# Kernel tuning notes

Hardware: AMD Instinct MI355X
Metric: run time of the kernel (lower is better)

Reference implementation:

```python
import jax, jax.numpy as jnp
import numpy as np

INPUT_DIM = 64
HIDDEN_DIM = 32


def setup_inputs() -> dict:
    key = jax.random.key(0)
    ks = jax.random.split(key, 9)
    B, C, H, W = 8, INPUT_DIM, 64, 64
    s_in = 1.0 / np.sqrt(C)
    inp = {
        "h": jax.random.normal(ks[0], (B, C, H, W), dtype=jnp.float32),
        # 1x1 conv weights stored as [out, in]
        "wq": jax.random.uniform(ks[1], (HIDDEN_DIM, C), jnp.float32, -s_in, s_in),
        "bq": jax.random.uniform(ks[2], (HIDDEN_DIM,), jnp.float32, -s_in, s_in),
        "wk": jax.random.uniform(ks[3], (HIDDEN_DIM, C), jnp.float32, -s_in, s_in),
        "bk": jax.random.uniform(ks[4], (HIDDEN_DIM,), jnp.float32, -s_in, s_in),
        "wv": jax.random.uniform(ks[5], (C, C), jnp.float32, -s_in, s_in),
        "bv": jax.random.uniform(ks[6], (C,), jnp.float32, -s_in, s_in),
        "wz": jax.random.uniform(ks[7], (C, C), jnp.float32, -s_in, s_in),
        "bz": jax.random.uniform(ks[8], (C,), jnp.float32, -s_in, s_in),
    }
    return inp


def reference(h, wq, bq, wk, bk, wv, bv, wz, bz):
    B, C, H, W = h.shape
    N = H * W
    x = h.reshape(B, C, N)  # [B, C, N]
    # 1x1 convs == channel-wise linear maps
    q = jnp.einsum('oc,bcn->bno', wq, x) + bq          # [B, N, Dh]
    k = jnp.einsum('oc,bcn->bon', wk, x) + bk[:, None]  # [B, Dh, N]
    v = jnp.einsum('oc,bcn->bon', wv, x) + bv[:, None]  # [B, C, N]
    attn = jax.nn.softmax(jnp.einsum('bnd,bdm->bnm', q, k), axis=-1)  # [B, N, N]
    z = jnp.einsum('bnm,bcm->bcn', attn, v)             # [B, C, N]
    out = jnp.einsum('oc,bcn->bon', wz, z) + bz[:, None]
    return out.reshape(B, C, H, W) + h
```

## Files before the change

kernel.cpp:

```cpp
#include <hip/hip_runtime.h>
#include <stdint.h>

#define BATCH 8
#define CIN   64
#define DH    32
#define NTOK  4096
#define LOG2E 1.4426950408889634f

typedef float    f4   __attribute__((ext_vector_type(4)));
typedef short    s8v  __attribute__((ext_vector_type(8)));
typedef uint32_t u32;
typedef uint32_t u32x2 __attribute__((ext_vector_type(2)));
typedef uint32_t u32x4 __attribute__((ext_vector_type(4)));

static __device__ __forceinline__ short f2bf(float f) {
    union { float f; u32 u; } c; c.f = f;
    u32 u = c.u;
    u32 r = (u + 0x7fffu + ((u >> 16) & 1u)) >> 16;
    return (short)(r & 0xffffu);
}
static __device__ __forceinline__ u32 pk2(float a, float b) {
    return (u32)(uint16_t)f2bf(a) | ((u32)(uint16_t)f2bf(b) << 16);
}
static __device__ __forceinline__ u32 pktr(float a, float b) {
    union { float f; u32 u; } ca, cb; ca.f = a; cb.f = b;
#if __has_builtin(__builtin_amdgcn_perm)
    return __builtin_amdgcn_perm(cb.u, ca.u, 0x07060302u);
#else
    return (cb.u & 0xffff0000u) | (ca.u >> 16);
#endif
}
static __device__ __forceinline__ float bfhi(u32 u) {
    union { u32 u; float f; } c; c.u = u & 0xffff0000u; return c.f;
}
static __device__ __forceinline__ float bflo(u32 u) {
    union { u32 u; float f; } c; c.u = u << 16; return c.f;
}

__global__ __launch_bounds__(256) void proj_kernel(
    const float* __restrict__ h,
    const float* __restrict__ wq, const float* __restrict__ bq,
    const float* __restrict__ wk, const float* __restrict__ bk,
    const float* __restrict__ wv, const float* __restrict__ bv,
    short* __restrict__ qbf, short* __restrict__ kbf, short* __restrict__ vp)
{
    __shared__ short xT [64 * 72];
    __shared__ short wqs[32 * 72];
    __shared__ short wks[32 * 72];
    __shared__ short wvs[64 * 72];
    __shared__ short vls2[64 * 68];
    __shared__ float bqs[32], bks[32], bvs[64];

    const int t   = threadIdx.x;
    const int b   = blockIdx.x;
    const int nt0 = blockIdx.y * 64;

    {
        const int c  = t >> 2;
        const int ng = (t & 3) * 16;
        const float* src = h + ((size_t)(b * CIN + c)) * NTOK + nt0 + ng;
        f4 x0 = *(const f4*)(src + 0);
        f4 x1 = *(const f4*)(src + 4);
        f4 x2 = *(const f4*)(src + 8);
        f4 x3 = *(const f4*)(src + 12);
        #pragma unroll
        for (int i = 0; i < 4; ++i) {
            xT[(ng + 0  + i) * 72 + c] = f2bf(x0[i]);
            xT[(ng + 4  + i) * 72 + c] = f2bf(x1[i]);
            xT[(ng + 8  + i) * 72 + c] = f2bf(x2[i]);
            xT[(ng + 12 + i) * 72 + c] = f2bf(x3[i]);
        }
    }
    for (int idx = t; idx < 2048; idx += 256) {
        int o = idx >> 6, c = idx & 63;
        wqs[o * 72 + c] = f2bf(wq[idx] * LOG2E);
        wks[o * 72 + c] = f2bf(wk[idx]);
    }
    for (int idx = t; idx < 4096; idx += 256)
        wvs[(idx >> 6) * 72 + (idx & 63)] = f2bf(wv[idx]);
    if (t < 32) { bqs[t] = bq[t] * LOG2E; bks[t] = bk[t]; }
    if (t < 64) bvs[t] = bv[t];
    __syncthreads();

    const int w    = t >> 6;
    const int ln   = t & 15;
    const int quad = (t >> 4) & 3;
    const int nl   = w * 16 + ln;
    const int n    = nt0 + nl;
    const f4 zf4 = {0.f, 0.f, 0.f, 0.f};

    const s8v xb0 = *(const s8v*)&xT[nl * 72 + quad * 8];
    const s8v xb1 = *(const s8v*)&xT[nl * 72 + 32 + quad * 8];

    #pragma unroll
    for (int ot = 0; ot < 2; ++ot) {
        s8v a0 = *(const s8v*)&wqs[(ot * 16 + ln) * 72 + quad * 8];
        s8v a1 = *(const s8v*)&wqs[(ot * 16 + ln) * 72 + 32 + quad * 8];
        f4 d = __builtin_amdgcn_mfma_f32_16x16x32_bf16(a0, xb0, zf4, 0, 0, 0);
        d     = __builtin_amdgcn_mfma_f32_16x16x32_bf16(a1, xb1, d,  0, 0, 0);
        f4 bb = *(const f4*)&bqs[ot * 16 + quad * 4];
        u32x2 pw; pw[0] = pk2(d[0] + bb[0], d[1] + bb[1]);
                  pw[1] = pk2(d[2] + bb[2], d[3] + bb[3]);
        *(u32x2*)(qbf + ((size_t)(b * NTOK + n)) * DH + ot * 16 + quad * 4) = pw;

        s8v c0 = *(const s8v*)&wks[(ot * 16 + ln) * 72 + quad * 8];
        s8v c1 = *(const s8v*)&wks[(ot * 16 + ln) * 72 + 32 + quad * 8];
        f4 e = __builtin_amdgcn_mfma_f32_16x16x32_bf16(c0, xb0, zf4, 0, 0, 0);
        e     = __builtin_amdgcn_mfma_f32_16x16x32_bf16(c1, xb1, e,  0, 0, 0);
        f4 kb = *(const f4*)&bks[ot * 16 + quad * 4];
        u32x2 kw; kw[0] = pk2(e[0] + kb[0], e[1] + kb[1]);
                  kw[1] = pk2(e[2] + kb[2], e[3] + kb[3]);
        *(u32x2*)(kbf + ((size_t)(b * NTOK + n)) * DH + ot * 16 + quad * 4) = kw;
    }

    {
        const int p    = nl & 31;
        const int row  = (nl >> 5) * 32 + ((p >> 2) & 3) * 8
                       + (p >> 4) * 4 + (p & 3);
        short* vrow = &vls2[row * 68];
        #pragma unroll
        for (int ot = 0; ot < 4; ++ot) {
            s8v a0 = *(const s8v*)&wvs[(ot * 16 + ln) * 72 + quad * 8];
            s8v a1 = *(const s8v*)&wvs[(ot * 16 + ln) * 72 + 32 + quad * 8];
            f4 d = __builtin_amdgcn_mfma_f32_16x16x32_bf16(a0, xb0, zf4, 0, 0, 0);
            d     = __builtin_amdgcn_mfma_f32_16x16x32_bf16(a1, xb1, d,  0, 0, 0);
            const int ch = ot * 16 + quad * 4;
            u32x2 pw;
            pw[0] = pk2(d[0] + bvs[ch],     d[1] + bvs[ch + 1]);
            pw[1] = pk2(d[2] + bvs[ch + 2], d[3] + bvs[ch + 3]);
            *(u32x2*)&vrow[ch] = pw;
        }
    }
    __syncthreads();

    {
        const int g = t >> 5;
        const int r = t & 31;
        short tmp[16];
        #pragma unroll
        for (int j = 0; j < 8; ++j)
            #pragma unroll
            for (int cc = 0; cc < 2; ++cc)
                tmp[cc * 8 + j] = vls2[(g * 8 + j) * 68 + r * 2 + cc];
        u32x4* dst = (u32x4*)(vp + ((size_t)(b * 128 + blockIdx.y * 2) * 4) * 64 * 8);
        #pragma unroll
        for (int i = 0; i < 2; ++i)
            dst[t * 2 + i] = ((const u32x4*)tmp)[i];
    }
}

__global__ __launch_bounds__(256, 2) void attn_kernel(
    const float* __restrict__ h,  const float* __restrict__ wz,
    const float* __restrict__ bz,
    const short* __restrict__ qbf, const short* __restrict__ kbf,
    const short* __restrict__ vp,  float* __restrict__ out)
{
    __shared__ short accb[4][64][72];
    __shared__ short zbuf[64][72];
    __shared__ float lbuf[4][64];

    const int b    = blockIdx.x;
    const int qb0  = blockIdx.y * 64;
    const int tid  = threadIdx.x;
    const int w    = tid >> 6;
    const int lane = tid & 63;
    const int ln   = lane & 15;
    const int quad = lane >> 4;
    const f4 zf4 = {0.f, 0.f, 0.f, 0.f};

    s8v qf[4];
    #pragma unroll
    for (int f = 0; f < 4; ++f)
        qf[f] = *(const s8v*)(qbf + ((size_t)(b * NTOK + qb0 + f * 16 + ln)) * DH + quad * 8);

    f4 acc[4][4];
    f4 accl[4];
    #pragma unroll
    for (int f = 0; f < 4; ++f) {
        accl[f] = zf4;
        #pragma unroll
        for (int ct = 0; ct < 4; ++ct) acc[f][ct] = zf4;
    }
    s8v ones;
    #pragma unroll
    for (int j = 0; j < 8; ++j) ones[j] = (short)0x3F80;

    const short* kb2 = kbf + ((size_t)b * NTOK + w * 1024) * DH;
    const s8v*   vb2 = (const s8v*)(vp + (size_t)b * NTOK * CIN)
                     + (size_t)(w * 32) * 4 * 64;

    for (int kt = 0; kt < 1024; kt += 32) {
        const short* kp = kb2 + kt * DH;
        s8v kk0 = *(const s8v*)(kp + ln * DH + quad * 8);
        s8v kk1 = *(const s8v*)(kp + (16 + ln) * DH + quad * 8);
        const s8v* vg = vb2 + (size_t)((kt >> 5) * 4 + quad) * 64 + ln;
        s8v v0 = vg[0], v1 = vg[16], v2 = vg[32], v3 = vg[48];

        #pragma unroll
        for (int f = 0; f < 4; ++f) {
            f4 sa = __builtin_amdgcn_mfma_f32_16x16x32_bf16(kk0, qf[f], zf4, 0, 0, 0);
            f4 sb = __builtin_amdgcn_mfma_f32_16x16x32_bf16(kk1, qf[f], zf4, 0, 0, 0);
            f4 ea, eb;
            #pragma unroll
            for (int r = 0; r < 4; ++r) {
                ea[r] = __builtin_amdgcn_exp2f(sa[r]);
                eb[r] = __builtin_amdgcn_exp2f(sb[r]);
            }
            u32x4 pd;
            pd[0] = pktr(ea[0], ea[1]); pd[1] = pktr(ea[2], ea[3]);
            pd[2] = pktr(eb[0], eb[1]); pd[3] = pktr(eb[2], eb[3]);
            s8v pf = __builtin_bit_cast(s8v, pd);

            accl[f]   = __builtin_amdgcn_mfma_f32_16x16x32_bf16(ones, pf, accl[f],   0, 0, 0);
            acc[f][0] = __builtin_amdgcn_mfma_f32_16x16x32_bf16(v0,   pf, acc[f][0], 0, 0, 0);
            acc[f][1] = __builtin_amdgcn_mfma_f32_16x16x32_bf16(v1,   pf, acc[f][1], 0, 0, 0);
            acc[f][2] = __builtin_amdgcn_mfma_f32_16x16x32_bf16(v2,   pf, acc[f][2], 0, 0, 0);
            acc[f][3] = __builtin_amdgcn_mfma_f32_16x16x32_bf16(v3,   pf, acc[f][3], 0, 0, 0);
        }
    }

    if (quad == 0) {
        #pragma unroll
        for (int f = 0; f < 4; ++f) lbuf[w][f * 16 + ln] = accl[f][0];
    }
    #pragma unroll
    for (int f = 0; f < 4; ++f) {
        #pragma unroll
        for (int ct = 0; ct < 4; ++ct) {
            u32x2 pw;
            pw[0] = pk2(acc[f][ct][0], acc[f][ct][1]);
            pw[1] = pk2(acc[f][ct][2], acc[f][ct][3]);
            *(u32x2*)&accb[w][f * 16 + ln][ct * 16 + quad * 4] = pw;
        }
    }
    __syncthreads();

    {
        const int q   = tid >> 2;
        const int chg = (tid & 3) * 16;
        float ls = lbuf[0][q] + lbuf[1][q] + lbuf[2][q] + lbuf[3][q];
        float rl = __builtin_amdgcn_rcpf(ls);
        float zv[16];
        #pragma unroll
        for (int i = 0; i < 16; ++i) zv[i] = 0.f;
        #pragma unroll
        for (int w2 = 0; w2 < 4; ++w2) {
            u32x4 ua = *(u32x4*)&accb[w2][q][chg];
            u32x4 ub = *(u32x4*)&accb[w2][q][chg + 8];
            #pragma unroll
            for (int d = 0; d < 4; ++d) {
                zv[d * 2]     += bflo(ua[d]); zv[d * 2 + 1]     += bfhi(ua[d]);
                zv[8 + d * 2] += bflo(ub[d]); zv[8 + d * 2 + 1] += bfhi(ub[d]);
            }
        }
        u32x4 za, zb2;
        #pragma unroll
        for (int d = 0; d < 4; ++d) {
            za[d]  = pk2(zv[d * 2] * rl,     zv[d * 2 + 1] * rl);
            zb2[d] = pk2(zv[8 + d * 2] * rl, zv[8 + d * 2 + 1] * rl);
        }
        *(u32x4*)&zbuf[q][chg]     = za;
        *(u32x4*)&zbuf[q][chg + 8] = zb2;
    }
    __syncthreads();

    {
        const int ot = w;
        s8v wzf[2];
        #pragma unroll
        for (int half = 0; half < 2; ++half) {
            const float* wp = wz + (ot * 16 + ln) * 64 + half * 32 + quad * 8;
            f4 wa = *(const f4*)wp;
            f4 wb = *(const f4*)(wp + 4);
            u32x4 tt;
            tt[0] = pk2(wa[0], wa[1]); tt[1] = pk2(wa[2], wa[3]);
            tt[2] = pk2(wb[0], wb[1]); tt[3] = pk2(wb[2], wb[3]);
            wzf[half] = __builtin_bit_cast(s8v, tt);
        }
        f4 bzv = *(const f4*)(bz + ot * 16 + quad * 4);
        #pragma unroll
        for (int fi = 0; fi < 4; ++fi) {
            const int row = fi * 16 + ln;
            s8v z0 = *(const s8v*)&zbuf[row][quad * 8];
            s8v z1 = *(const s8v*)&zbuf[row][32 + quad * 8];
            f4 oa = __builtin_amdgcn_mfma_f32_16x16x32_bf16(wzf[0], z0, zf4, 0, 0, 0);
            oa     = __builtin_amdgcn_mfma_f32_16x16x32_bf16(wzf[1], z1, oa,  0, 0, 0);
            #pragma unroll
            for (int r = 0; r < 4; ++r) {
                size_t idx = ((size_t)(b * CIN + ot * 16 + quad * 4 + r)) * NTOK
                           + qb0 + row;
                out[idx] = oa[r] + bzv[r] + h[idx];
            }
        }
    }
}

extern "C" void kernel_launch(void* const* d_in, const int* in_sizes, int n_in,
                              void* d_out, int out_size, void* d_ws, size_t ws_size,
                              hipStream_t stream) {
    (void)in_sizes; (void)n_in; (void)out_size; (void)ws_size;
    const float* h  = (const float*)d_in[0];
    const float* wq = (const float*)d_in[1];
    const float* bq = (const float*)d_in[2];
    const float* wk = (const float*)d_in[3];
    const float* bk = (const float*)d_in[4];
    const float* wv = (const float*)d_in[5];
    const float* bv = (const float*)d_in[6];
    const float* wz = (const float*)d_in[7];
    const float* bz = (const float*)d_in[8];
    float* out = (float*)d_out;

    short* qbf = (short*)d_ws;
    short* kbf = qbf + (size_t)BATCH * NTOK * DH;
    short* vpw = kbf + (size_t)BATCH * NTOK * DH;

    proj_kernel<<<dim3(8, 64), dim3(256), 0, stream>>>(
        h, wq, bq, wk, bk, wv, bv, qbf, kbf, vpw);
    attn_kernel<<<dim3(8, 64), dim3(256), 0, stream>>>(
        h, wz, bz, qbf, kbf, vpw, out);
}
```

Before: 117.2 us.

## Double-buffer K/V register loads in attention loop and vectorize weight staging

```diff
diff --git a/kernel.cpp b/kernel.cpp
--- a/kernel.cpp
+++ b/kernel.cpp
@@ -71,13 +71,24 @@
             xT[(ng + 12 + i) * 72 + c] = f2bf(x3[i]);
         }
     }
-    for (int idx = t; idx < 2048; idx += 256) {
-        int o = idx >> 6, c = idx & 63;
-        wqs[o * 72 + c] = f2bf(wq[idx] * LOG2E);
-        wks[o * 72 + c] = f2bf(wk[idx]);
-    }
-    for (int idx = t; idx < 4096; idx += 256)
-        wvs[(idx >> 6) * 72 + (idx & 63)] = f2bf(wv[idx]);
+    #pragma unroll
+    for (int idx = t; idx < 512; idx += 256) {
+        f4 a = *(const f4*)(wq + idx * 4);
+        f4 c = *(const f4*)(wk + idx * 4);
+        const int o = idx >> 4, cc = (idx & 15) * 4;
+        u32x2 qa; qa[0] = pk2(a[0] * LOG2E, a[1] * LOG2E);
+                  qa[1] = pk2(a[2] * LOG2E, a[3] * LOG2E);
+        u32x2 ka; ka[0] = pk2(c[0], c[1]); ka[1] = pk2(c[2], c[3]);
+        *(u32x2*)&wqs[o * 72 + cc] = qa;
+        *(u32x2*)&wks[o * 72 + cc] = ka;
+    }
+    #pragma unroll
+    for (int idx = t; idx < 1024; idx += 256) {
+        f4 a = *(const f4*)(wv + idx * 4);
+        const int o = idx >> 4, cc = (idx & 15) * 4;
+        u32x2 va; va[0] = pk2(a[0], a[1]); va[1] = pk2(a[2], a[3]);
+        *(u32x2*)&wvs[o * 72 + cc] = va;
+    }
     if (t < 32) { bqs[t] = bq[t] * LOG2E; bks[t] = bk[t]; }
     if (t < 64) bvs[t] = bv[t];
     __syncthreads();
@@ -149,6 +160,47 @@
     }
 }
 
+static __device__ __forceinline__ void load_kv(
+    const short* __restrict__ kb2, const s8v* __restrict__ vb2,
+    int kt, int ln, int quad,
+    s8v& kk0, s8v& kk1, s8v& v0, s8v& v1, s8v& v2, s8v& v3)
+{
+    const short* kp = kb2 + kt * DH;
+    kk0 = *(const s8v*)(kp + ln * DH + quad * 8);
+    kk1 = *(const s8v*)(kp + (16 + ln) * DH + quad * 8);
+    const s8v* vg = vb2 + (size_t)((kt >> 5) * 4 + quad) * 64 + ln;
+    v0 = vg[0]; v1 = vg[16]; v2 = vg[32]; v3 = vg[48];
+}
+
+static __device__ __forceinline__ void attn_step(
+    const s8v& kk0, const s8v& kk1,
+    const s8v& v0, const s8v& v1, const s8v& v2, const s8v& v3,
+    const s8v (&qf)[4], const s8v& ones, f4 (&acc)[4][4], f4 (&accl)[4])
+{
+    const f4 zf4 = {0.f, 0.f, 0.f, 0.f};
+    #pragma unroll
+    for (int f = 0; f < 4; ++f) {
+        f4 sa = __builtin_amdgcn_mfma_f32_16x16x32_bf16(kk0, qf[f], zf4, 0, 0, 0);
+        f4 sb = __builtin_amdgcn_mfma_f32_16x16x32_bf16(kk1, qf[f], zf4, 0, 0, 0);
+        f4 ea, eb;
+        #pragma unroll
+        for (int r = 0; r < 4; ++r) {
+            ea[r] = __builtin_amdgcn_exp2f(sa[r]);
+            eb[r] = __builtin_amdgcn_exp2f(sb[r]);
+        }
+        u32x4 pd;
+        pd[0] = pktr(ea[0], ea[1]); pd[1] = pktr(ea[2], ea[3]);
+        pd[2] = pktr(eb[0], eb[1]); pd[3] = pktr(eb[2], eb[3]);
+        s8v pf = __builtin_bit_cast(s8v, pd);
+
+        accl[f]   = __builtin_amdgcn_mfma_f32_16x16x32_bf16(ones, pf, accl[f],   0, 0, 0);
+        acc[f][0] = __builtin_amdgcn_mfma_f32_16x16x32_bf16(v0,   pf, acc[f][0], 0, 0, 0);
+        acc[f][1] = __builtin_amdgcn_mfma_f32_16x16x32_bf16(v1,   pf, acc[f][1], 0, 0, 0);
+        acc[f][2] = __builtin_amdgcn_mfma_f32_16x16x32_bf16(v2,   pf, acc[f][2], 0, 0, 0);
+        acc[f][3] = __builtin_amdgcn_mfma_f32_16x16x32_bf16(v3,   pf, acc[f][3], 0, 0, 0);
+    }
+}
+
 __global__ __launch_bounds__(256, 2) void attn_kernel(
     const float* __restrict__ h,  const float* __restrict__ wz,
     const float* __restrict__ bz,
@@ -189,34 +241,21 @@
     const s8v*   vb2 = (const s8v*)(vp + (size_t)b * NTOK * CIN)
                      + (size_t)(w * 32) * 4 * 64;
 
-    for (int kt = 0; kt < 1024; kt += 32) {
-        const short* kp = kb2 + kt * DH;
-        s8v kk0 = *(const s8v*)(kp + ln * DH + quad * 8);
-        s8v kk1 = *(const s8v*)(kp + (16 + ln) * DH + quad * 8);
-        const s8v* vg = vb2 + (size_t)((kt >> 5) * 4 + quad) * 64 + ln;
-        s8v v0 = vg[0], v1 = vg[16], v2 = vg[32], v3 = vg[48];
-
-        #pragma unroll
-        for (int f = 0; f < 4; ++f) {
-            f4 sa = __builtin_amdgcn_mfma_f32_16x16x32_bf16(kk0, qf[f], zf4, 0, 0, 0);
-            f4 sb = __builtin_amdgcn_mfma_f32_16x16x32_bf16(kk1, qf[f], zf4, 0, 0, 0);
-            f4 ea, eb;
-            #pragma unroll
-            for (int r = 0; r < 4; ++r) {
-                ea[r] = __builtin_amdgcn_exp2f(sa[r]);
-                eb[r] = __builtin_amdgcn_exp2f(sb[r]);
-            }
-            u32x4 pd;
-            pd[0] = pktr(ea[0], ea[1]); pd[1] = pktr(ea[2], ea[3]);
-            pd[2] = pktr(eb[0], eb[1]); pd[3] = pktr(eb[2], eb[3]);
-            s8v pf = __builtin_bit_cast(s8v, pd);
-
-            accl[f]   = __builtin_amdgcn_mfma_f32_16x16x32_bf16(ones, pf, accl[f],   0, 0, 0);
-            acc[f][0] = __builtin_amdgcn_mfma_f32_16x16x32_bf16(v0,   pf, acc[f][0], 0, 0, 0);
-            acc[f][1] = __builtin_amdgcn_mfma_f32_16x16x32_bf16(v1,   pf, acc[f][1], 0, 0, 0);
-            acc[f][2] = __builtin_amdgcn_mfma_f32_16x16x32_bf16(v2,   pf, acc[f][2], 0, 0, 0);
-            acc[f][3] = __builtin_amdgcn_mfma_f32_16x16x32_bf16(v3,   pf, acc[f][3], 0, 0, 0);
-        }
+    s8v kA0, kA1, vA0, vA1, vA2, vA3;
+    s8v kB0, kB1, vB0, vB1, vB2, vB3;
+    load_kv(kb2, vb2, 0, ln, quad, kA0, kA1, vA0, vA1, vA2, vA3);
+
+    for (int kt = 0; kt < 1024; kt += 64) {
+        load_kv(kb2, vb2, kt + 32, ln, quad, kB0, kB1, vB0, vB1, vB2, vB3);
+        __builtin_amdgcn_s_setprio(1);
+        attn_step(kA0, kA1, vA0, vA1, vA2, vA3, qf, ones, acc, accl);
+        __builtin_amdgcn_s_setprio(0);
+
+        if (kt < 960)
+            load_kv(kb2, vb2, kt + 64, ln, quad, kA0, kA1, vA0, vA1, vA2, vA3);
+        __builtin_amdgcn_s_setprio(1);
+        attn_step(kB0, kB1, vB0, vB1, vB2, vB3, qf, ones, acc, accl);
+        __builtin_amdgcn_s_setprio(0);
     }
 
     if (quad == 0) {
```

Result: faster. 112.0 us (-4.5%).
